# Kernel tuning notes

Hardware: AMD Instinct MI355X
Metric: run time of the kernel (lower is better)

Reference implementation:

```python
import jax, jax.numpy as jnp
import numpy as np
import math

N, DM, DK, DV, KWIN = 500, 2048, 2048, 2048, 10

def _xavier(key, shape):
    fan_out, fan_in = shape[0], shape[1]
    limit = math.sqrt(6.0 / (fan_in + fan_out))
    return jax.random.uniform(key, (shape[0], shape[1]), jnp.float32, -limit, limit)

def setup_inputs() -> dict:
    key = jax.random.key(0)
    ks = jax.random.split(key, 7)
    X = jax.random.normal(ks[0], (N, DM), jnp.float32)
    mask = jax.random.randint(ks[1], (N, N), 0, 2, jnp.int32)
    # torch Linear weight is (out, in); store transposed so fwd is X @ W
    Wq = _xavier(ks[2], (DK, DM)).T  # [DM, DK]
    Wk = _xavier(ks[3], (DK, DM)).T
    Wv = _xavier(ks[4], (DV, DM)).T
    Wo = _xavier(ks[5], (DM, DV)).T  # [DV, DM]
    wk = _xavier(ks[6], (2 * KWIN + 1, DM))  # relative-position embedding table
    return {"X": X, "mask": mask, "Wq": Wq, "Wk": Wk, "Wv": Wv, "Wo": Wo, "wk": wk}

def reference(X, mask, Wq, Wk, Wv, Wo, wk):
    n = X.shape[0]
    scale = 1.0 / math.sqrt(DK)
    Q = X @ Wq            # [n, dk]
    K = X @ Wk            # [n, dk]
    V = X @ Wv            # [n, dv]
    Qs = Q * scale
    S = Qs @ K.T          # [n, n] content scores
    # relative-position bias: Sr[i,j] = Qs[i] . wk[clip(j-i,-k,k)+k]
    # (Shaw-style gather; identical math to wk[table] matmul, no [n,n,dm] intermediate)
    idx = jnp.clip(jnp.arange(n)[None, :] - jnp.arange(n)[:, None], -KWIN, KWIN) + KWIN  # [n, n]
    QR = Qs @ wk.T                                   # [n, 2k+1]
    Sr = jnp.take_along_axis(QR, idx, axis=1)        # [n, n]
    S = S + Sr
    S = jnp.where(mask == 0, jnp.float32(-1e9), S)
    A = jax.nn.softmax(S, axis=-1)                   # dropout_rate=0 -> identity
    Y = (A @ V) @ Wo                                 # [n, dm]
    return (Y, A)
```

## Files before the change

### kernel.cpp

```cpp
#include <hip/hip_runtime.h>
#include <hip/hip_bf16.h>


#define N_TOK 500
#define MP 512
#define DM 2048
#define KWIN_ 10
#define NREL 21

typedef __hip_bfloat16 bf16;
typedef __attribute__((ext_vector_type(8))) short short8;
typedef __attribute__((ext_vector_type(4))) float floatx4;

#define NS 262144L

__device__ inline float bfj(const short8& v, int j) {
  return __bfloat162float(((const bf16*)&v)[j]);
}

__device__ __forceinline__ void gload16(const bf16* g, bf16* l) {
  __builtin_amdgcn_global_load_lds(
      (const __attribute__((address_space(1))) void*)g,
      (__attribute__((address_space(3))) void*)l, 16, 0, 0);
}

__global__ __launch_bounds__(256) void prep(
    const float* __restrict__ Wq, const float* __restrict__ Wk,
    const float* __restrict__ Wv, const float* __restrict__ Wo,
    const float* __restrict__ X, const float* __restrict__ wk,
    bf16* __restrict__ WqkT, bf16* __restrict__ WvT, bf16* __restrict__ WoT,
    bf16* __restrict__ Xb, bf16* __restrict__ wkb) {
  int z = blockIdx.z;
  int tid = threadIdx.x;
  if (z == 4) {
    int row = blockIdx.y * 32 + blockIdx.x;
    int c0 = tid * 8;
    bf16 v[8];
    if (row < MP) {
      if (row < N_TOK) {
        const float* p = X + (long)row * DM + c0;
#pragma unroll
        for (int j = 0; j < 8; ++j) v[j] = __float2bfloat16(p[j]);
      } else {
#pragma unroll
        for (int j = 0; j < 8; ++j) v[j] = __float2bfloat16(0.f);
      }
      *(short8*)(Xb + (long)row * DM + c0) = *(short8*)v;
    } else if (row < MP + NREL) {
      int r = row - MP;
      const float* p = wk + (long)r * DM + c0;
#pragma unroll
      for (int j = 0; j < 8; ++j) v[j] = __float2bfloat16(p[j]);
      *(short8*)(wkb + (long)r * DM + c0) = *(short8*)v;
    }
    return;
  }
  const float* W = (z == 0) ? Wq : (z == 1) ? Wk : (z == 2) ? Wv : Wo;
  bf16* Out = (z == 0) ? WqkT
            : (z == 1) ? (WqkT + (long)DM * DM)
            : (z == 2) ? WvT : WoT;
  __shared__ float t[64][68];
  int k0 = blockIdx.y * 64, n0 = blockIdx.x * 64;
  int rr = tid >> 4, cc = (tid & 15) * 4;
  int gsw = cc >> 2;
#pragma unroll
  for (int p = 0; p < 4; ++p) {
    int r = rr + 16 * p;
    float4 v = *(const float4*)(W + (long)(k0 + r) * DM + n0 + cc);
    *(float4*)&t[r][(gsw ^ (r & 3)) * 4] = v;
  }
  __syncthreads();
#pragma unroll
  for (int s0 = 0; s0 < 2; ++s0) {
    int s = tid + s0 * 256;
    int n = s >> 3, c = s & 7;
    bf16 v[8];
#pragma unroll
    for (int j = 0; j < 8; ++j) {
      int rowt = c * 8 + j;
      int col = ((n >> 2) ^ (rowt & 3)) * 4 + (n & 3);
      v[j] = __float2bfloat16(t[rowt][col]);
    }
    *(short8*)(Out + (long)(n0 + n) * DM + k0 + c * 8) = *(short8*)v;
  }
}

template <int BM, int OUT>
__device__ __forceinline__ void gemm_core(
    bf16* sm, const bf16* __restrict__ A, int lda, const bf16* __restrict__ B,
    int ldb, float* __restrict__ Cf, bf16* __restrict__ Cb, int ldc,
    int kStart, int kLen, int row0, int col0, int mLim) {
  constexpr int GM = (BM == 128) ? 4 : 2;
  constexpr int ROWS = BM + 128;
  constexpr int BUFE = ROWS * 32;
  int tid = threadIdx.x;
  int lane = tid & 63, w = tid >> 6;
  int l16 = lane & 15, l4 = lane >> 4;
  int lrow = lane >> 2;
  int lcol = ((lane & 3) ^ ((lane >> 3) & 3)) * 8;
  int wr = (w & 1) * (16 * GM), wc = (w >> 1) * 64;
  const bf16* Ab = A + (long)row0 * lda + kStart;
  const bf16* Bb = B + (long)col0 * ldb + kStart;
  const int arow0 = (BM == 128) ? 32 * w : 16 * w;
  const int brow0 = BM + 32 * w;
  const bf16* aSrc0 = Ab + (long)(arow0 + lrow) * lda + lcol;
  const bf16* aSrc1 = Ab + (long)(arow0 + 16 + lrow) * lda + lcol;
  const bf16* bSrc0 = Bb + (long)(32 * w + lrow) * ldb + lcol;
  const bf16* bSrc1 = Bb + (long)(32 * w + 16 + lrow) * ldb + lcol;

  floatx4 acc[GM][4] = {};
  int NT = kLen >> 5;

#define STAGE(buf, kk)                                                \
  do {                                                                \
    bf16* bp = sm + (buf) * BUFE;                                     \
    gload16(aSrc0 + (kk), bp + arow0 * 32);                           \
    if (BM == 128) gload16(aSrc1 + (kk), bp + (arow0 + 16) * 32);     \
    gload16(bSrc0 + (kk), bp + brow0 * 32);                           \
    gload16(bSrc1 + (kk), bp + (brow0 + 16) * 32);                    \
  } while (0)

  STAGE(0, 0);
  STAGE(1, 32);
  STAGE(2, 64);
  int rd = ((l16 >> 1) & 3) * 8;
  for (int t = 0; t < NT; ++t) {
    if (t + 3 < NT) {
      STAGE((t + 3) & 3, (t + 3) * 32);
      if (BM == 128)
        asm volatile("s_waitcnt vmcnt(12)" ::: "memory");
      else
        asm volatile("s_waitcnt vmcnt(9)" ::: "memory");
    } else {
      asm volatile("s_waitcnt vmcnt(0)" ::: "memory");
    }
    __builtin_amdgcn_s_barrier();
    __builtin_amdgcn_sched_barrier(0);
    const bf16* bp = sm + (t & 3) * BUFE;
    short8 af[GM], bg[4];
#pragma unroll
    for (int g = 0; g < GM; ++g)
      af[g] = *(const short8*)(bp + (wr + g * 16 + l16) * 32 + (l4 * 8 ^ rd));
#pragma unroll
    for (int h = 0; h < 4; ++h)
      bg[h] = *(const short8*)(bp + (BM + wc + h * 16 + l16) * 32 + (l4 * 8 ^ rd));
#pragma unroll
    for (int g = 0; g < GM; ++g)
#pragma unroll
      for (int h = 0; h < 4; ++h)
        acc[g][h] = __builtin_amdgcn_mfma_f32_16x16x32_bf16(af[g], bg[h],
                                                            acc[g][h], 0, 0, 0);
    __builtin_amdgcn_sched_barrier(0);
    asm volatile("s_waitcnt lgkmcnt(0)" ::: "memory");
    __builtin_amdgcn_s_barrier();
  }
#undef STAGE

#pragma unroll
  for (int g = 0; g < GM; ++g)
#pragma unroll
    for (int h = 0; h < 4; ++h)
#pragma unroll
      for (int i = 0; i < 4; ++i) {
        long r = row0 + wr + g * 16 + l4 * 4 + i;
        long c = col0 + wc + h * 16 + l16;
        if (r < mLim) {
          if (OUT == 0)
            Cf[r * ldc + c] = acc[g][h][i];
          else
            Cb[r * ldc + c] = __float2bfloat16(acc[g][h][i]);
        }
      }
}

__global__ __launch_bounds__(256, 2) void gemm_qkvt(
    const bf16* __restrict__ Xb, const bf16* __restrict__ WqkT,
    const bf16* __restrict__ WvT, bf16* __restrict__ QKbf,
    bf16* __restrict__ Vtb) {
  __shared__ __align__(16) bf16 sm[4 * 256 * 32];
  int id = blockIdx.x;
  if (id < 128) {
    int row0 = (id >> 5) * 128, col0 = (id & 31) * 128;
    gemm_core<128, 1>(sm, Xb, DM, WqkT, DM, nullptr, QKbf, 4096, 0, DM, row0,
                      col0, MP);
  } else {
    int t = id - 128;
    int row0 = (t >> 2) * 64, col0 = (t & 3) * 128;
    gemm_core<64, 1>(sm, WvT, DM, Xb, DM, nullptr, Vtb, MP, 0, DM, row0, col0,
                     DM);
  }
}

template <int BM, int OUT>
__global__ __launch_bounds__(256, 2) void gemm_k(
    const bf16* __restrict__ A, int lda, const bf16* __restrict__ B, int ldb,
    float* __restrict__ Cf, bf16* __restrict__ Cb, int ldc, int sliceK,
    long cstride, int mLim) {
  __shared__ __align__(16) bf16 sm[4 * (BM + 128) * 32];
  float* cf = (OUT == 0) ? Cf + (long)blockIdx.z * cstride : nullptr;
  gemm_core<BM, OUT>(sm, A, lda, B, ldb, cf, Cb, ldc, blockIdx.z * sliceK,
                     sliceK, blockIdx.y * BM, blockIdx.x * 128, mLim);
}

__global__ __launch_bounds__(256) void softmax_qr(
    const float* __restrict__ Sp, const bf16* __restrict__ QKbf,
    const bf16* __restrict__ wkb, const int* __restrict__ mask,
    float* __restrict__ Aout, bf16* __restrict__ Abf) {
  int i = blockIdx.x;
  int tid = threadIdx.x;
  if (i >= N_TOK) {
    Abf[(long)i * MP + tid] = __float2bfloat16(0.f);
    Abf[(long)i * MP + tid + 256] = __float2bfloat16(0.f);
    return;
  }
  int lane = tid & 63, w = tid >> 6;
  __shared__ float sQR[24];
  __shared__ float red[4];
  short8 q[4];
#pragma unroll
  for (int s = 0; s < 4; ++s)
    q[s] = *(const short8*)(QKbf + (long)i * 4096 + s * 512 + lane * 8);
  for (int r = w; r < NREL; r += 4) {
    float p = 0.f;
#pragma unroll
    for (int s = 0; s < 4; ++s) {
      short8 wv = *(const short8*)(wkb + (long)r * DM + s * 512 + lane * 8);
#pragma unroll
      for (int j = 0; j < 8; ++j) p += bfj(q[s], j) * bfj(wv, j);
    }
#pragma unroll
    for (int o = 32; o > 0; o >>= 1) p += __shfl_down(p, o);
    if (lane == 0) sQR[r] = p;
  }
  __syncthreads();
  const float scale = 0.022097086912079608f;
  float v0, v1 = -1e30f;
  int j0 = tid, j1 = tid + 256;
  {
    float s = 0.f;
#pragma unroll
    for (int z = 0; z < 8; ++z) s += Sp[z * NS + (long)i * MP + j0];
    int rel = j0 - i;
    rel = rel < -KWIN_ ? -KWIN_ : (rel > KWIN_ ? KWIN_ : rel);
    s = scale * (s + sQR[rel + KWIN_]);
    if (mask[(long)i * N_TOK + j0] == 0) s = -1e9f;
    v0 = s;
  }
  if (j1 < N_TOK) {
    float s = 0.f;
#pragma unroll
    for (int z = 0; z < 8; ++z) s += Sp[z * NS + (long)i * MP + j1];
    int rel = j1 - i;
    rel = rel < -KWIN_ ? -KWIN_ : (rel > KWIN_ ? KWIN_ : rel);
    s = scale * (s + sQR[rel + KWIN_]);
    if (mask[(long)i * N_TOK + j1] == 0) s = -1e9f;
    v1 = s;
  }
  float mx = fmaxf(v0, v1);
#pragma unroll
  for (int o = 32; o > 0; o >>= 1) mx = fmaxf(mx, __shfl_down(mx, o));
  if (lane == 0) red[w] = mx;
  __syncthreads();
  if (tid == 0) red[0] = fmaxf(fmaxf(red[0], red[1]), fmaxf(red[2], red[3]));
  __syncthreads();
  mx = red[0];
  __syncthreads();
  float e0 = expf(v0 - mx);
  float e1 = (j1 < N_TOK) ? expf(v1 - mx) : 0.f;
  float sum = e0 + e1;
#pragma unroll
  for (int o = 32; o > 0; o >>= 1) sum += __shfl_down(sum, o);
  if (lane == 0) red[w] = sum;
  __syncthreads();
  if (tid == 0) red[0] = red[0] + red[1] + red[2] + red[3];
  __syncthreads();
  float inv = 1.f / red[0];
  float a0 = e0 * inv, a1 = e1 * inv;
  Aout[(long)i * N_TOK + j0] = a0;
  if (j1 < N_TOK) Aout[(long)i * N_TOK + j1] = a1;
  Abf[(long)i * MP + j0] = __float2bfloat16(a0);
  Abf[(long)i * MP + j1] = __float2bfloat16(a1);
}

extern "C" void kernel_launch(void* const* d_in, const int* in_sizes, int n_in,
                              void* d_out, int out_size, void* d_ws,
                              size_t ws_size, hipStream_t stream) {
  const float* X = (const float*)d_in[0];
  const int* mask = (const int*)d_in[1];
  const float* Wq = (const float*)d_in[2];
  const float* Wk = (const float*)d_in[3];
  const float* Wv = (const float*)d_in[4];
  const float* Wo = (const float*)d_in[5];
  const float* wk = (const float*)d_in[6];

  float* Yout = (float*)d_out;
  float* Aout = Yout + (long)N_TOK * DM;

  const long MB = 1 << 20;
  char* p = (char*)d_ws;
  bf16* Xb = (bf16*)p;
  bf16* WqkT = (bf16*)(p + 2 * MB);
  bf16* WvT = (bf16*)(p + 18 * MB);
  bf16* WoT = (bf16*)(p + 26 * MB);
  bf16* wkb = (bf16*)(p + 34 * MB);
  bf16* QKbf = (bf16*)(p + 35 * MB);
  bf16* Vtb = (bf16*)(p + 39 * MB);
  float* Sp = (float*)(p + 41 * MB);
  bf16* Abf = (bf16*)(p + 49 * MB);
  bf16* AVbf = (bf16*)(p + 50 * MB);

  dim3 b256(256);

  prep<<<dim3(32, 32, 5), b256, 0, stream>>>(Wq, Wk, Wv, Wo, X, wk, WqkT, WvT,
                                             WoT, Xb, wkb);
  gemm_qkvt<<<dim3(256), b256, 0, stream>>>(Xb, WqkT, WvT, QKbf, Vtb);
  gemm_k<64, 0><<<dim3(4, 8, 8), b256, 0, stream>>>(
      QKbf, 4096, QKbf + 2048, 4096, Sp, nullptr, MP, 256, NS, MP);
  softmax_qr<<<dim3(MP), b256, 0, stream>>>(Sp, QKbf, wkb, mask, Aout, Abf);
  gemm_k<64, 1><<<dim3(16, 8, 1), b256, 0, stream>>>(
      Abf, MP, Vtb, MP, nullptr, AVbf, DM, MP, 0, MP);
  gemm_k<64, 0><<<dim3(16, 8, 1), b256, 0, stream>>>(
      AVbf, DM, WoT, DM, Yout, nullptr, DM, DM, 0, N_TOK);
}
```

Baseline: 178.8 us.

## Fuse all stages into one persistent kernel with atomic grid barriers

```diff
diff --git a/kernel.cpp b/kernel.cpp
--- a/kernel.cpp
+++ b/kernel.cpp
@@ -24,16 +24,31 @@
       (__attribute__((address_space(3))) void*)l, 16, 0, 0);
 }
 
-__global__ __launch_bounds__(256) void prep(
-    const float* __restrict__ Wq, const float* __restrict__ Wk,
-    const float* __restrict__ Wv, const float* __restrict__ Wo,
-    const float* __restrict__ X, const float* __restrict__ wk,
-    bf16* __restrict__ WqkT, bf16* __restrict__ WvT, bf16* __restrict__ WoT,
-    bf16* __restrict__ Xb, bf16* __restrict__ wkb) {
-  int z = blockIdx.z;
-  int tid = threadIdx.x;
+__device__ __forceinline__ void gridbar(unsigned* cnt, unsigned target) {
+  __syncthreads();
+  if (threadIdx.x == 0) {
+    __threadfence();
+    atomicAdd(cnt, 1u);
+    while (atomicAdd(cnt, 0u) < target) __builtin_amdgcn_s_sleep(16);
+    __threadfence();
+  }
+  __syncthreads();
+}
+
+__device__ void prep_unit(int u, int tid, char* smraw,
+                          const float* __restrict__ Wq,
+                          const float* __restrict__ Wk,
+                          const float* __restrict__ Wv,
+                          const float* __restrict__ Wo,
+                          const float* __restrict__ X,
+                          const float* __restrict__ wk, bf16* __restrict__ WqkT,
+                          bf16* __restrict__ WvT, bf16* __restrict__ WoT,
+                          bf16* __restrict__ Xb, bf16* __restrict__ wkb) {
+  int z = u >> 10;
+  int rem = u & 1023;
+  int bx = rem & 31, by = rem >> 5;
   if (z == 4) {
-    int row = blockIdx.y * 32 + blockIdx.x;
+    int row = by * 32 + bx;
     int c0 = tid * 8;
     bf16 v[8];
     if (row < MP) {
@@ -59,8 +74,9 @@
   bf16* Out = (z == 0) ? WqkT
             : (z == 1) ? (WqkT + (long)DM * DM)
             : (z == 2) ? WvT : WoT;
-  __shared__ float t[64][68];
-  int k0 = blockIdx.y * 64, n0 = blockIdx.x * 64;
+  float(*t)[68] = (float(*)[68])smraw;
+  __syncthreads();
+  int k0 = by * 64, n0 = bx * 64;
   int rr = tid >> 4, cc = (tid & 15) * 4;
   int gsw = cc >> 2;
 #pragma unroll
@@ -111,13 +127,13 @@
   floatx4 acc[GM][4] = {};
   int NT = kLen >> 5;
 
-#define STAGE(buf, kk)                                                \
-  do {                                                                \
-    bf16* bp = sm + (buf) * BUFE;                                     \
-    gload16(aSrc0 + (kk), bp + arow0 * 32);                           \
-    if (BM == 128) gload16(aSrc1 + (kk), bp + (arow0 + 16) * 32);     \
-    gload16(bSrc0 + (kk), bp + brow0 * 32);                           \
-    gload16(bSrc1 + (kk), bp + (brow0 + 16) * 32);                    \
+#define STAGE(buf, kk)                                            \
+  do {                                                            \
+    bf16* bp = sm + (buf) * BUFE;                                 \
+    gload16(aSrc0 + (kk), bp + arow0 * 32);                       \
+    if (BM == 128) gload16(aSrc1 + (kk), bp + (arow0 + 16) * 32); \
+    gload16(bSrc0 + (kk), bp + brow0 * 32);                       \
+    gload16(bSrc1 + (kk), bp + (brow0 + 16) * 32);                \
   } while (0)
 
   STAGE(0, 0);
@@ -143,7 +159,8 @@
       af[g] = *(const short8*)(bp + (wr + g * 16 + l16) * 32 + (l4 * 8 ^ rd));
 #pragma unroll
     for (int h = 0; h < 4; ++h)
-      bg[h] = *(const short8*)(bp + (BM + wc + h * 16 + l16) * 32 + (l4 * 8 ^ rd));
+      bg[h] =
+          *(const short8*)(bp + (BM + wc + h * 16 + l16) * 32 + (l4 * 8 ^ rd));
 #pragma unroll
     for (int g = 0; g < GM; ++g)
 #pragma unroll
@@ -173,49 +190,20 @@
       }
 }
 
-__global__ __launch_bounds__(256, 2) void gemm_qkvt(
-    const bf16* __restrict__ Xb, const bf16* __restrict__ WqkT,
-    const bf16* __restrict__ WvT, bf16* __restrict__ QKbf,
-    bf16* __restrict__ Vtb) {
-  __shared__ __align__(16) bf16 sm[4 * 256 * 32];
-  int id = blockIdx.x;
-  if (id < 128) {
-    int row0 = (id >> 5) * 128, col0 = (id & 31) * 128;
-    gemm_core<128, 1>(sm, Xb, DM, WqkT, DM, nullptr, QKbf, 4096, 0, DM, row0,
-                      col0, MP);
-  } else {
-    int t = id - 128;
-    int row0 = (t >> 2) * 64, col0 = (t & 3) * 128;
-    gemm_core<64, 1>(sm, WvT, DM, Xb, DM, nullptr, Vtb, MP, 0, DM, row0, col0,
-                     DM);
-  }
-}
-
-template <int BM, int OUT>
-__global__ __launch_bounds__(256, 2) void gemm_k(
-    const bf16* __restrict__ A, int lda, const bf16* __restrict__ B, int ldb,
-    float* __restrict__ Cf, bf16* __restrict__ Cb, int ldc, int sliceK,
-    long cstride, int mLim) {
-  __shared__ __align__(16) bf16 sm[4 * (BM + 128) * 32];
-  float* cf = (OUT == 0) ? Cf + (long)blockIdx.z * cstride : nullptr;
-  gemm_core<BM, OUT>(sm, A, lda, B, ldb, cf, Cb, ldc, blockIdx.z * sliceK,
-                     sliceK, blockIdx.y * BM, blockIdx.x * 128, mLim);
-}
-
-__global__ __launch_bounds__(256) void softmax_qr(
-    const float* __restrict__ Sp, const bf16* __restrict__ QKbf,
-    const bf16* __restrict__ wkb, const int* __restrict__ mask,
-    float* __restrict__ Aout, bf16* __restrict__ Abf) {
-  int i = blockIdx.x;
-  int tid = threadIdx.x;
+__device__ void softmax_row(int i, int tid, char* smraw,
+                            const float* __restrict__ Sp,
+                            const bf16* __restrict__ QKbf,
+                            const bf16* __restrict__ wkb,
+                            const int* __restrict__ mask,
+                            float* __restrict__ Aout, bf16* __restrict__ Abf) {
   if (i >= N_TOK) {
     Abf[(long)i * MP + tid] = __float2bfloat16(0.f);
     Abf[(long)i * MP + tid + 256] = __float2bfloat16(0.f);
     return;
   }
   int lane = tid & 63, w = tid >> 6;
-  __shared__ float sQR[24];
-  __shared__ float red[4];
+  float* sQR = (float*)smraw;
+  float* red = (float*)smraw + 24;
   short8 q[4];
 #pragma unroll
   for (int s = 0; s < 4; ++s)
@@ -280,6 +268,64 @@
   if (j1 < N_TOK) Aout[(long)i * N_TOK + j1] = a1;
   Abf[(long)i * MP + j0] = __float2bfloat16(a0);
   Abf[(long)i * MP + j1] = __float2bfloat16(a1);
+}
+
+__global__ __launch_bounds__(256) void fused(
+    const float* __restrict__ X, const int* __restrict__ mask,
+    const float* __restrict__ Wq, const float* __restrict__ Wk,
+    const float* __restrict__ Wv, const float* __restrict__ Wo,
+    const float* __restrict__ wk, bf16* __restrict__ WqkT,
+    bf16* __restrict__ WvT, bf16* __restrict__ WoT, bf16* __restrict__ Xb,
+    bf16* __restrict__ wkb, bf16* __restrict__ QKbf, bf16* __restrict__ Vtb,
+    float* __restrict__ Sp, bf16* __restrict__ Abf, bf16* __restrict__ AVbf,
+    float* __restrict__ Yout, float* __restrict__ Aout,
+    unsigned* __restrict__ cnt) {
+  __shared__ __align__(16) char smraw[65536];
+  bf16* sm = (bf16*)smraw;
+  int bid = blockIdx.x, tid = threadIdx.x;
+
+  for (int u = 0; u < 20; ++u)
+    prep_unit(bid * 20 + u, tid, smraw, Wq, Wk, Wv, Wo, X, wk, WqkT, WvT, WoT,
+              Xb, wkb);
+  gridbar(cnt, 256);
+
+  if (bid < 128) {
+    int row0 = (bid >> 5) * 128, col0 = (bid & 31) * 128;
+    gemm_core<128, 1>(sm, Xb, DM, WqkT, DM, nullptr, QKbf, 4096, 0, DM, row0,
+                      col0, MP);
+  } else {
+    int t = bid - 128;
+    int row0 = (t >> 2) * 64, col0 = (t & 3) * 128;
+    gemm_core<64, 1>(sm, WvT, DM, Xb, DM, nullptr, Vtb, MP, 0, DM, row0, col0,
+                     DM);
+  }
+  gridbar(cnt, 512);
+
+  {
+    int x = bid & 3, y = (bid >> 2) & 7, z = bid >> 5;
+    gemm_core<64, 0>(sm, QKbf, 4096, QKbf + 2048, 4096, Sp + (long)z * NS,
+                     nullptr, MP, z * 256, 256, y * 64, x * 128, MP);
+  }
+  gridbar(cnt, 768);
+
+  for (int r = 0; r < 2; ++r) {
+    __syncthreads();
+    softmax_row(bid + r * 256, tid, smraw, Sp, QKbf, wkb, mask, Aout, Abf);
+  }
+  gridbar(cnt, 1024);
+
+  if (bid < 128) {
+    int row0 = (bid >> 4) * 64, col0 = (bid & 15) * 128;
+    gemm_core<64, 1>(sm, Abf, MP, Vtb, MP, nullptr, AVbf, DM, 0, MP, row0,
+                     col0, MP);
+  }
+  gridbar(cnt, 1280);
+
+  if (bid < 128) {
+    int row0 = (bid >> 4) * 64, col0 = (bid & 15) * 128;
+    gemm_core<64, 0>(sm, AVbf, DM, WoT, DM, Yout, nullptr, DM, 0, DM, row0,
+                     col0, N_TOK);
+  }
 }
 
 extern "C" void kernel_launch(void* const* d_in, const int* in_sizes, int n_in,
@@ -308,17 +354,10 @@
   float* Sp = (float*)(p + 41 * MB);
   bf16* Abf = (bf16*)(p + 49 * MB);
   bf16* AVbf = (bf16*)(p + 50 * MB);
-
-  dim3 b256(256);
-
-  prep<<<dim3(32, 32, 5), b256, 0, stream>>>(Wq, Wk, Wv, Wo, X, wk, WqkT, WvT,
-                                             WoT, Xb, wkb);
-  gemm_qkvt<<<dim3(256), b256, 0, stream>>>(Xb, WqkT, WvT, QKbf, Vtb);
-  gemm_k<64, 0><<<dim3(4, 8, 8), b256, 0, stream>>>(
-      QKbf, 4096, QKbf + 2048, 4096, Sp, nullptr, MP, 256, NS, MP);
-  softmax_qr<<<dim3(MP), b256, 0, stream>>>(Sp, QKbf, wkb, mask, Aout, Abf);
-  gemm_k<64, 1><<<dim3(16, 8, 1), b256, 0, stream>>>(
-      Abf, MP, Vtb, MP, nullptr, AVbf, DM, MP, 0, MP);
-  gemm_k<64, 0><<<dim3(16, 8, 1), b256, 0, stream>>>(
-      AVbf, DM, WoT, DM, Yout, nullptr, DM, DM, 0, N_TOK);
-}
+  unsigned* cnt = (unsigned*)(p + 96 * MB);
+
+  hipMemsetAsync(cnt, 0, 64, stream);
+  fused<<<dim3(256), dim3(256), 0, stream>>>(X, mask, Wq, Wk, Wv, Wo, wk, WqkT,
+                                             WvT, WoT, Xb, wkb, QKbf, Vtb, Sp,
+                                             Abf, AVbf, Yout, Aout, cnt);
+}
```

Result: slower. 298.6 us (+67.1%).

## Widen GEMM K-tile to 64 with triple-buffered LDS pipeline

Applied to the files above, without the earlier changes.

```diff
diff --git a/kernel.cpp b/kernel.cpp
--- a/kernel.cpp
+++ b/kernel.cpp
@@ -91,68 +91,77 @@
     int ldb, float* __restrict__ Cf, bf16* __restrict__ Cb, int ldc,
     int kStart, int kLen, int row0, int col0, int mLim) {
   constexpr int GM = (BM == 128) ? 4 : 2;
-  constexpr int ROWS = BM + 128;
-  constexpr int BUFE = ROWS * 32;
+  constexpr int AISS = (BM == 128) ? 4 : 2;
+  constexpr int LPT = AISS + 4;
+  constexpr int BUFE = (BM + 128) * 64;
   int tid = threadIdx.x;
   int lane = tid & 63, w = tid >> 6;
   int l16 = lane & 15, l4 = lane >> 4;
-  int lrow = lane >> 2;
-  int lcol = ((lane & 3) ^ ((lane >> 3) & 3)) * 8;
+  int srow = lane >> 3;
+  int scol = ((lane & 7) ^ srow) * 8;
   int wr = (w & 1) * (16 * GM), wc = (w >> 1) * 64;
+  const int arow0 = (BM == 128) ? 32 * w : 16 * w;
+  const int brow0 = BM + 32 * w;
   const bf16* Ab = A + (long)row0 * lda + kStart;
   const bf16* Bb = B + (long)col0 * ldb + kStart;
-  const int arow0 = (BM == 128) ? 32 * w : 16 * w;
-  const int brow0 = BM + 32 * w;
-  const bf16* aSrc0 = Ab + (long)(arow0 + lrow) * lda + lcol;
-  const bf16* aSrc1 = Ab + (long)(arow0 + 16 + lrow) * lda + lcol;
-  const bf16* bSrc0 = Bb + (long)(32 * w + lrow) * ldb + lcol;
-  const bf16* bSrc1 = Bb + (long)(32 * w + 16 + lrow) * ldb + lcol;
+  const bf16* aP[AISS];
+  const bf16* bP[4];
+#pragma unroll
+  for (int a = 0; a < AISS; ++a)
+    aP[a] = Ab + (long)(arow0 + a * 8 + srow) * lda + scol;
+#pragma unroll
+  for (int b = 0; b < 4; ++b)
+    bP[b] = Bb + (long)(32 * w + b * 8 + srow) * ldb + scol;
 
   floatx4 acc[GM][4] = {};
-  int NT = kLen >> 5;
-
-#define STAGE(buf, kk)                                                \
-  do {                                                                \
-    bf16* bp = sm + (buf) * BUFE;                                     \
-    gload16(aSrc0 + (kk), bp + arow0 * 32);                           \
-    if (BM == 128) gload16(aSrc1 + (kk), bp + (arow0 + 16) * 32);     \
-    gload16(bSrc0 + (kk), bp + brow0 * 32);                           \
-    gload16(bSrc1 + (kk), bp + (brow0 + 16) * 32);                    \
+  int NT = kLen >> 6;
+
+#define STAGE(buf, kk)                                              \
+  do {                                                              \
+    bf16* bp_ = sm + (buf) * BUFE;                                  \
+    _Pragma("unroll") for (int a_ = 0; a_ < AISS; ++a_)             \
+        gload16(aP[a_] + (kk), bp_ + (arow0 + a_ * 8) * 64);        \
+    _Pragma("unroll") for (int b_ = 0; b_ < 4; ++b_)                \
+        gload16(bP[b_] + (kk), bp_ + (brow0 + b_ * 8) * 64);        \
   } while (0)
 
   STAGE(0, 0);
-  STAGE(1, 32);
-  STAGE(2, 64);
-  int rd = ((l16 >> 1) & 3) * 8;
+  if (NT > 1) STAGE(1, 64);
+  int bufr = 0, bufw = 2;
+  int sw = l16 & 7;
   for (int t = 0; t < NT; ++t) {
-    if (t + 3 < NT) {
-      STAGE((t + 3) & 3, (t + 3) * 32);
-      if (BM == 128)
-        asm volatile("s_waitcnt vmcnt(12)" ::: "memory");
-      else
-        asm volatile("s_waitcnt vmcnt(9)" ::: "memory");
+    if (t + 2 < NT) {
+      STAGE(bufw, (t + 2) * 64);
+      asm volatile("s_waitcnt vmcnt(%0)" ::"n"(2 * LPT) : "memory");
     } else {
       asm volatile("s_waitcnt vmcnt(0)" ::: "memory");
     }
     __builtin_amdgcn_s_barrier();
     __builtin_amdgcn_sched_barrier(0);
-    const bf16* bp = sm + (t & 3) * BUFE;
-    short8 af[GM], bg[4];
-#pragma unroll
-    for (int g = 0; g < GM; ++g)
-      af[g] = *(const short8*)(bp + (wr + g * 16 + l16) * 32 + (l4 * 8 ^ rd));
-#pragma unroll
-    for (int h = 0; h < 4; ++h)
-      bg[h] = *(const short8*)(bp + (BM + wc + h * 16 + l16) * 32 + (l4 * 8 ^ rd));
-#pragma unroll
-    for (int g = 0; g < GM; ++g)
-#pragma unroll
-      for (int h = 0; h < 4; ++h)
-        acc[g][h] = __builtin_amdgcn_mfma_f32_16x16x32_bf16(af[g], bg[h],
-                                                            acc[g][h], 0, 0, 0);
+    const bf16* bp = sm + bufr * BUFE;
+#pragma unroll
+    for (int h = 0; h < 2; ++h) {
+      short8 af[GM], bg[4];
+#pragma unroll
+      for (int g = 0; g < GM; ++g)
+        af[g] = *(const short8*)(bp + (wr + g * 16 + l16) * 64 +
+                                 ((h * 4 + l4) ^ sw) * 8);
+#pragma unroll
+      for (int h2 = 0; h2 < 4; ++h2)
+        bg[h2] = *(const short8*)(bp + (BM + wc + h2 * 16 + l16) * 64 +
+                                  ((h * 4 + l4) ^ sw) * 8);
+#pragma unroll
+      for (int g = 0; g < GM; ++g)
+#pragma unroll
+        for (int h2 = 0; h2 < 4; ++h2)
+          acc[g][h2] = __builtin_amdgcn_mfma_f32_16x16x32_bf16(
+              af[g], bg[h2], acc[g][h2], 0, 0, 0);
+    }
     __builtin_amdgcn_sched_barrier(0);
     asm volatile("s_waitcnt lgkmcnt(0)" ::: "memory");
     __builtin_amdgcn_s_barrier();
+    bufr = (bufr == 2) ? 0 : bufr + 1;
+    bufw = (bufw == 2) ? 0 : bufw + 1;
   }
 #undef STAGE
 
@@ -173,11 +182,11 @@
       }
 }
 
-__global__ __launch_bounds__(256, 2) void gemm_qkvt(
+__global__ __launch_bounds__(256) void gemm_qkvt(
     const bf16* __restrict__ Xb, const bf16* __restrict__ WqkT,
     const bf16* __restrict__ WvT, bf16* __restrict__ QKbf,
     bf16* __restrict__ Vtb) {
-  __shared__ __align__(16) bf16 sm[4 * 256 * 32];
+  __shared__ __align__(16) bf16 sm[3 * 256 * 64];
   int id = blockIdx.x;
   if (id < 128) {
     int row0 = (id >> 5) * 128, col0 = (id & 31) * 128;
@@ -191,15 +200,15 @@
   }
 }
 
-template <int BM, int OUT>
+template <int OUT>
 __global__ __launch_bounds__(256, 2) void gemm_k(
     const bf16* __restrict__ A, int lda, const bf16* __restrict__ B, int ldb,
     float* __restrict__ Cf, bf16* __restrict__ Cb, int ldc, int sliceK,
     long cstride, int mLim) {
-  __shared__ __align__(16) bf16 sm[4 * (BM + 128) * 32];
+  __shared__ __align__(16) bf16 sm[3 * 192 * 64];
   float* cf = (OUT == 0) ? Cf + (long)blockIdx.z * cstride : nullptr;
-  gemm_core<BM, OUT>(sm, A, lda, B, ldb, cf, Cb, ldc, blockIdx.z * sliceK,
-                     sliceK, blockIdx.y * BM, blockIdx.x * 128, mLim);
+  gemm_core<64, OUT>(sm, A, lda, B, ldb, cf, Cb, ldc, blockIdx.z * sliceK,
+                     sliceK, blockIdx.y * 64, blockIdx.x * 128, mLim);
 }
 
 __global__ __launch_bounds__(256) void softmax_qr(
@@ -314,11 +323,11 @@
   prep<<<dim3(32, 32, 5), b256, 0, stream>>>(Wq, Wk, Wv, Wo, X, wk, WqkT, WvT,
                                              WoT, Xb, wkb);
   gemm_qkvt<<<dim3(256), b256, 0, stream>>>(Xb, WqkT, WvT, QKbf, Vtb);
-  gemm_k<64, 0><<<dim3(4, 8, 8), b256, 0, stream>>>(
+  gemm_k<0><<<dim3(4, 8, 8), b256, 0, stream>>>(
       QKbf, 4096, QKbf + 2048, 4096, Sp, nullptr, MP, 256, NS, MP);
   softmax_qr<<<dim3(MP), b256, 0, stream>>>(Sp, QKbf, wkb, mask, Aout, Abf);
-  gemm_k<64, 1><<<dim3(16, 8, 1), b256, 0, stream>>>(
+  gemm_k<1><<<dim3(16, 8, 1), b256, 0, stream>>>(
       Abf, MP, Vtb, MP, nullptr, AVbf, DM, MP, 0, MP);
-  gemm_k<64, 0><<<dim3(16, 8, 1), b256, 0, stream>>>(
+  gemm_k<0><<<dim3(16, 8, 1), b256, 0, stream>>>(
       AVbf, DM, WoT, DM, Yout, nullptr, DM, DM, 0, N_TOK);
 }
```

New measurement: 173.8 us. 1.03x faster.
